# Kernel tuning notes

Measured on AMD Instinct MI355X. Metric: run time of the kernel, lower is better.

## Reference

```python
import jax, jax.numpy as jnp
import numpy as np

B, T, H, K = 64, 1024, 256, 4  # batch, seq_len, hidden_dim, crf_size


def setup_inputs() -> dict:
    key = jax.random.key(0)
    ks = jax.random.split(key, 8)
    return {
        "sentence_features": jax.random.normal(ks[0], (B, T, H), dtype=jnp.float32),
        "conv_w": jax.random.normal(ks[1], (H, H, 3), dtype=jnp.float32) * (1.0 / np.sqrt(3 * H)),
        "conv_b": jnp.zeros((H,), dtype=jnp.float32),
        "lin_w": jax.random.normal(ks[2], (K, H), dtype=jnp.float32) * (1.0 / np.sqrt(H)),
        "lin_b": jnp.zeros((K,), dtype=jnp.float32),
        "crf_start": jax.random.uniform(ks[3], (K,), dtype=jnp.float32, minval=-0.1, maxval=0.1),
        "crf_end": jax.random.uniform(ks[4], (K,), dtype=jnp.float32, minval=-0.1, maxval=0.1),
        "crf_trans": jax.random.uniform(ks[5], (K, K), dtype=jnp.float32, minval=-0.1, maxval=0.1),
    }


def _emissions(x, conv_w, conv_b, lin_w, lin_b):
    # x: [B, T, H] -> transpose -> Conv1d(k=3, pad=1) -> ReLU -> transpose -> Linear
    xc = jnp.swapaxes(x, 1, 2)  # [B, H, T]
    y = jax.lax.conv_general_dilated(
        xc, conv_w, window_strides=(1,), padding=((1, 1),),
        dimension_numbers=("NCH", "OIH", "NCH"))
    y = jax.nn.relu(y + conv_b[None, :, None])
    y = jnp.swapaxes(y, 1, 2)  # [B, T, H]
    return y @ lin_w.T + lin_b  # [B, T, K]


def _viterbi_decode(em, start, end, trans):
    # em: [B, T, K]; torchcrf CRF.decode with no mask (batch_first=True)
    score0 = start[None, :] + em[:, 0]  # [B, K]

    def step(score, emit_t):
        # score [B, K] over prev tag; broadcast to [B, K_prev, K_next]
        nxt = score[:, :, None] + trans[None, :, :] + emit_t[:, None, :]
        return jnp.max(nxt, axis=1), jnp.argmax(nxt, axis=1)  # new score, best prev tag

    em_rest = jnp.swapaxes(em[:, 1:], 0, 1)  # [T-1, B, K]
    final, history = jax.lax.scan(step, score0, em_rest)
    final = final + end[None, :]
    last_tag = jnp.argmax(final, axis=-1)  # [B]

    def back(tag, idx_t):
        prev = jnp.take_along_axis(idx_t, tag[:, None], axis=1)[:, 0]
        return prev, prev

    _, tags_head = jax.lax.scan(back, last_tag, history, reverse=True)  # [T-1, B]
    path = jnp.concatenate([jnp.swapaxes(tags_head, 0, 1), last_tag[:, None]], axis=1)
    return path.astype(jnp.int32)  # [B, T]


def reference(sentence_features, conv_w, conv_b, lin_w, lin_b, crf_start, crf_end, crf_trans):
    em = _emissions(sentence_features, conv_w, conv_b, lin_w, lin_b)
    return _viterbi_decode(em, crf_start, crf_end, crf_trans)
```

## Files before the change

kernel.cpp:

```cpp
#include <hip/hip_runtime.h>
#include <cstdint>
#include <cstddef>

typedef __attribute__((ext_vector_type(8))) short short8;
typedef __attribute__((ext_vector_type(4))) float f32x4;

constexpr int Bn = 64, Tn = 1024, Hn = 256, Kn = 4;
constexpr int TT = 128;
constexpr int AROWS = TT + 2;
constexpr int ARSTR = 144;

__device__ __forceinline__ unsigned bf16rne(float f) {
  unsigned u = __float_as_uint(f);
  return (u + 0x7fffu + ((u >> 16) & 1u)) >> 16;
}

__global__ __launch_bounds__(256) void pack_b_k(const float* __restrict__ conv_w,
                                                unsigned short* __restrict__ Bp) {
  int gt = blockIdx.x * 256 + threadIdx.x;
  int fid = gt >> 6, l = gt & 63;
  int ks = fid >> 5, rem = fid & 31;
  int p = rem >> 4, nf = rem & 15;
  int n = nf * 16 + (l & 15);
  int k0 = ks * 32 + ((l >> 4) << 3);
  short8 s;
  #pragma unroll
  for (int j = 0; j < 8; ++j) {
    int k = k0 + j;
    int dt = k >> 8, i = k & 255;
    float w = conv_w[n * 768 + i * 3 + dt];
    unsigned hb = bf16rne(w);
    if (p == 0) s[j] = (short)hb;
    else        s[j] = (short)bf16rne(w - __uint_as_float(hb << 16));
  }
  *reinterpret_cast<short8*>(Bp + (size_t)fid * 512 + l * 8) = s;
}

__global__ __launch_bounds__(256, 3) void emis_k(const float* __restrict__ x,
    const unsigned short* __restrict__ Bp, const float* __restrict__ conv_b,
    const float* __restrict__ lin_w, float* __restrict__ em2) {
  __shared__ __align__(16) char A_lds[AROWS * ARSTR];

  const int b = blockIdx.z, ny = blockIdx.y, t0 = blockIdx.x * TT;
  const int tid = threadIdx.x, lane = tid & 63, w = tid >> 6;
  const int wm = w >> 1, wn = w & 1;
  const float* xb = x + (size_t)b * Tn * Hn;

  auto stageA = [&](int ig) {
    #pragma unroll 1
    for (int it = 0; it < 5; ++it) {
      int idx = it * 256 + tid;
      if (idx < AROWS * 8) {
        int row = idx >> 3, c4 = idx & 7;
        int trow = t0 - 1 + row;
        float4 v = make_float4(0.f, 0.f, 0.f, 0.f);
        if (trow >= 0 && trow < Tn)
          v = *reinterpret_cast<const float4*>(xb + (size_t)trow * Hn + ig * 32 + c4 * 4);
        unsigned h[4], lo[4];
        float vf[4] = {v.x, v.y, v.z, v.w};
        #pragma unroll
        for (int q = 0; q < 4; ++q) {
          h[q] = bf16rne(vf[q]);
          lo[q] = bf16rne(vf[q] - __uint_as_float(h[q] << 16));
        }
        uint2 hp, lp;
        hp.x = h[0] | (h[1] << 16);  hp.y = h[2] | (h[3] << 16);
        lp.x = lo[0] | (lo[1] << 16); lp.y = lo[2] | (lo[3] << 16);
        char* base = A_lds + row * ARSTR + c4 * 8;
        *reinterpret_cast<uint2*>(base) = hp;
        *reinterpret_cast<uint2*>(base + 64) = lp;
      }
    }
  };

  const char* bsrc = reinterpret_cast<const char*>(Bp)
      + (size_t)(ny * 8 + wn * 4) * 1024 + lane * 16;
  auto loadB = [&](short8* Bh, short8* Bl, int ks) {
    #pragma unroll
    for (int nf = 0; nf < 4; ++nf) {
      Bh[nf] = *reinterpret_cast<const short8*>(bsrc + (size_t)((ks * 2 + 0) * 16 + nf) * 1024);
      Bl[nf] = *reinterpret_cast<const short8*>(bsrc + (size_t)((ks * 2 + 1) * 16 + nf) * 1024);
    }
  };

  f32x4 acc[4][4];
  #pragma unroll
  for (int mf = 0; mf < 4; ++mf)
    #pragma unroll
    for (int nf = 0; nf < 4; ++nf) acc[mf][nf] = (f32x4)0.f;

  const char* aB = A_lds + (lane & 15) * ARSTR + ((lane >> 4) << 4) + wm * 64 * ARSTR;

#define STEP(DT, BH, BL, NBH, NBL, KSN)                                       \
  {                                                                           \
    loadB(NBH, NBL, (KSN));                                                   \
    __builtin_amdgcn_s_setprio(1);                                            \
    _Pragma("unroll")                                                         \
    for (int mf = 0; mf < 4; ++mf) {                                          \
      const char* ap = aB + (mf * 16 + (DT)) * ARSTR;                         \
      short8 Ah = *reinterpret_cast<const short8*>(ap);                       \
      short8 Al = *reinterpret_cast<const short8*>(ap + 64);                  \
      _Pragma("unroll")                                                       \
      for (int nf = 0; nf < 4; ++nf) {                                        \
        f32x4 c = acc[mf][nf];                                                \
        c = __builtin_amdgcn_mfma_f32_16x16x32_bf16(Ah, BH[nf], c, 0, 0, 0);  \
        c = __builtin_amdgcn_mfma_f32_16x16x32_bf16(Al, BH[nf], c, 0, 0, 0);  \
        c = __builtin_amdgcn_mfma_f32_16x16x32_bf16(Ah, BL[nf], c, 0, 0, 0);  \
        acc[mf][nf] = c;                                                      \
      }                                                                       \
    }                                                                         \
    __builtin_amdgcn_s_setprio(0);                                            \
  }

  short8 BhA[4], BlA[4], BhB[4], BlB[4];
  loadB(BhA, BlA, 0);
  stageA(0);
  __syncthreads();

  #pragma unroll 1
  for (int igp = 0; igp < 4; ++igp) {
    const int ig0 = igp * 2, ig1 = ig0 + 1;
    STEP(0, BhA, BlA, BhB, BlB, 8 + ig0);
    STEP(1, BhB, BlB, BhA, BlA, 16 + ig0);
    STEP(2, BhA, BlA, BhB, BlB, ig1);
    __syncthreads();
    stageA(ig1);
    __syncthreads();
    STEP(0, BhB, BlB, BhA, BlA, 8 + ig1);
    STEP(1, BhA, BlA, BhB, BlB, 16 + ig1);
    STEP(2, BhB, BlB, BhA, BlA, (ig1 < 7 ? ig1 + 1 : 0));
    if (igp < 3) {
      __syncthreads();
      stageA(ig1 + 1);
      __syncthreads();
    }
  }
#undef STEP

  f32x4 pem[4][4];
  #pragma unroll
  for (int mf = 0; mf < 4; ++mf)
    #pragma unroll
    for (int v = 0; v < 4; ++v) pem[mf][v] = (f32x4)0.f;

  #pragma unroll
  for (int nf = 0; nf < 4; ++nf) {
    const int gcol = ny * 128 + wn * 64 + nf * 16 + (lane & 15);
    const float cb = conv_b[gcol];
    f32x4 lw;
    lw[0] = lin_w[gcol]; lw[1] = lin_w[256 + gcol];
    lw[2] = lin_w[512 + gcol]; lw[3] = lin_w[768 + gcol];
    #pragma unroll
    for (int mf = 0; mf < 4; ++mf)
      #pragma unroll
      for (int v = 0; v < 4; ++v) {
        float val = fmaxf(acc[mf][nf][v] + cb, 0.f);
        pem[mf][v] += val * lw;
      }
  }
  #pragma unroll
  for (int mf = 0; mf < 4; ++mf)
    #pragma unroll
    for (int v = 0; v < 4; ++v) {
      f32x4 t = pem[mf][v];
      #pragma unroll
      for (int m = 1; m < 16; m <<= 1) {
        f32x4 q;
        q[0] = __shfl_xor(t[0], m); q[1] = __shfl_xor(t[1], m);
        q[2] = __shfl_xor(t[2], m); q[3] = __shfl_xor(t[3], m);
        t += q;
      }
      pem[mf][v] = t;
    }
  __syncthreads();
  float* red = reinterpret_cast<float*>(A_lds);
  if ((lane & 15) == 0) {
    const int g = lane >> 4;
    #pragma unroll
    for (int mf = 0; mf < 4; ++mf)
      #pragma unroll
      for (int v = 0; v < 4; ++v) {
        int r = wm * 64 + mf * 16 + g * 4 + v;
        *reinterpret_cast<f32x4*>(red + (r * 2 + wn) * 4) = pem[mf][v];
      }
  }
  __syncthreads();
  if (tid < 128) {
    f32x4 s0 = *reinterpret_cast<f32x4*>(red + tid * 8);
    f32x4 s1 = *reinterpret_cast<f32x4*>(red + tid * 8 + 4);
    f32x4 s = s0 + s1;
    *reinterpret_cast<f32x4*>(em2 + ((size_t)(b * Tn + t0 + tid) * 2 + ny) * 4) = s;
  }
}

__device__ __forceinline__ unsigned int compose_map(unsigned int a, unsigned int b) {
#if __has_builtin(__builtin_amdgcn_perm)
  return __builtin_amdgcn_perm(a, a, b);
#else
  unsigned int c = 0;
  #pragma unroll
  for (int k = 0; k < 4; ++k) {
    unsigned int sel = (b >> (8 * k)) & 0xffu;
    c |= ((a >> (8 * sel)) & 0xffu) << (8 * k);
  }
  return c;
#endif
}

template <int J>
__device__ __forceinline__ float qb(float v) {
  return __int_as_float(__builtin_amdgcn_update_dpp(
      0, __float_as_int(v), (J * 0x55), 0xf, 0xf, true));
}

#define PSTEP(EV, T)                                                       \
  {                                                                        \
    shf[((T) - 1) * 4 + kk] = s;                                           \
    float c0 = qb<0>(s) + trc0;                                            \
    float c1 = qb<1>(s) + trc1;                                            \
    float c2 = qb<2>(s) + trc2;                                            \
    float c3 = qb<3>(s) + trc3;                                            \
    s = fmaxf(fmaxf(c0, c1), fmaxf(c2, c3)) + (EV);                        \
  }

__global__ __launch_bounds__(64) void viterbi_k(const float* __restrict__ em2,
    const float* __restrict__ lin_b, const float* __restrict__ cstart,
    const float* __restrict__ cend, const float* __restrict__ ctrans,
    int* __restrict__ out) {
  __shared__ float4 se[Tn];
  __shared__ float4 sh[Tn - 1];
  __shared__ int s_last;
  const int b = blockIdx.x, lane = threadIdx.x;
  const float4* e2 = reinterpret_cast<const float4*>(em2 + (size_t)b * Tn * 8);
  const float lb0 = lin_b[0], lb1 = lin_b[1], lb2 = lin_b[2], lb3 = lin_b[3];
  for (int i = lane; i < Tn; i += 64) {
    float4 a = e2[i * 2], c = e2[i * 2 + 1];
    se[i] = make_float4(a.x + c.x + lb0, a.y + c.y + lb1,
                        a.z + c.z + lb2, a.w + c.w + lb3);
  }
  float tr[4][4];
  #pragma unroll
  for (int j = 0; j < 4; ++j)
    #pragma unroll
    for (int k = 0; k < 4; ++k) tr[j][k] = ctrans[j * 4 + k];
  __syncthreads();

  if (lane < 4) {
    const int kk = lane;
    const float* sef = reinterpret_cast<const float*>(se);
    float* shf = reinterpret_cast<float*>(sh);
    const float trc0 = ctrans[0 * 4 + kk];
    const float trc1 = ctrans[1 * 4 + kk];
    const float trc2 = ctrans[2 * 4 + kk];
    const float trc3 = ctrans[3 * 4 + kk];
    float s = cstart[kk] + sef[kk];
    float e[8];
    #pragma unroll
    for (int d = 0; d < 8; ++d) e[d] = sef[(1 + d) * 4 + kk];
    int t = 1;
    #pragma unroll 1
    for (int g = 0; g < 127; ++g, t += 8) {
      float f[8];
      #pragma unroll
      for (int d = 0; d < 8; ++d) f[d] = e[d];
      #pragma unroll
      for (int d = 0; d < 8; ++d) e[d] = sef[(t + 8 + d) * 4 + kk];
      PSTEP(f[0], t);     PSTEP(f[1], t + 1);
      PSTEP(f[2], t + 2); PSTEP(f[3], t + 3);
      PSTEP(f[4], t + 4); PSTEP(f[5], t + 5);
      PSTEP(f[6], t + 6); PSTEP(f[7], t + 7);
    }
    PSTEP(e[0], 1017); PSTEP(e[1], 1018); PSTEP(e[2], 1019);
    PSTEP(e[3], 1020); PSTEP(e[4], 1021); PSTEP(e[5], 1022);
    PSTEP(e[6], 1023);
    s += cend[kk];
    float f0 = __shfl(s, 0), f1 = __shfl(s, 1);
    float f2 = __shfl(s, 2), f3 = __shfl(s, 3);
    if (kk == 0) {
      int tag = 0; float bf = f0;
      if (f1 > bf) { bf = f1; tag = 1; }
      if (f2 > bf) { bf = f2; tag = 2; }
      if (f3 > bf) { bf = f3; tag = 3; }
      s_last = tag;
    }
  }
  __syncthreads();

  const unsigned int ID = 0x03020100u;
  unsigned int mloc[16];
  const int t0 = lane * 16;
  #pragma unroll
  for (int k = 0; k < 16; ++k) {
    const int t = t0 + k;
    if (t < Tn - 1) {
      const float4 s = sh[t];
      const float4 e = se[t + 1];
      const float sj[4] = {s.x, s.y, s.z, s.w};
      const float ev[4] = {e.x, e.y, e.z, e.w};
      unsigned int mw = 0;
      #pragma unroll
      for (int kk = 0; kk < 4; ++kk) {
        float best = (sj[0] + tr[0][kk]) + ev[kk];
        int bi = 0;
        #pragma unroll
        for (int j = 1; j < 4; ++j) {
          float cc = (sj[j] + tr[j][kk]) + ev[kk];
          if (cc > best) { best = cc; bi = j; }
        }
        mw |= (unsigned)bi << (8 * kk);
      }
      mloc[k] = mw;
    } else {
      mloc[k] = ID;
    }
  }
  unsigned int P = mloc[15];
  #pragma unroll
  for (int k = 14; k >= 0; --k) P = compose_map(mloc[k], P);
  #pragma unroll
  for (int d = 1; d < 64; d <<= 1) {
    unsigned int q = (unsigned int)__shfl_down((int)P, d);
    if (lane + d > 63) q = ID;
    P = compose_map(P, q);
  }
  unsigned int E = (unsigned int)__shfl_down((int)P, 1);
  if (lane == 63) E = ID;
  const int last = s_last;
  unsigned int tag = (E >> (8 * last)) & 3u;
  int* ob = out + (size_t)b * Tn;
  #pragma unroll
  for (int k = 15; k >= 0; --k) {
    tag = (mloc[k] >> (8 * tag)) & 3u;
    ob[t0 + k] = (int)tag;
  }
}

extern "C" void kernel_launch(void* const* d_in, const int* in_sizes, int n_in,
                              void* d_out, int out_size, void* d_ws, size_t ws_size,
                              hipStream_t stream) {
  const float* x      = (const float*)d_in[0];
  const float* conv_w = (const float*)d_in[1];
  const float* conv_b = (const float*)d_in[2];
  const float* lin_w  = (const float*)d_in[3];
  const float* lin_b  = (const float*)d_in[4];
  const float* cstart = (const float*)d_in[5];
  const float* cend   = (const float*)d_in[6];
  const float* ctrans = (const float*)d_in[7];
  int* out = (int*)d_out;

  unsigned short* Bp = (unsigned short*)d_ws;
  float* em2 = (float*)((char*)d_ws + 786432);

  pack_b_k<<<192, 256, 0, stream>>>(conv_w, Bp);
  emis_k<<<dim3(Tn / TT, 2, Bn), 256, 0, stream>>>(x, Bp, conv_b, lin_w, em2);
  viterbi_k<<<Bn, 64, 0, stream>>>(em2, lin_b, cstart, cend, ctrans, out);
}
```

Before: 134.0 us.

## Double-buffer A tile in LDS and prefetch next slab into registers

Splits A staging into a global-to-register prefetch issued before the MFMA steps and a later register-to-LDS write into a second LDS buffer. This lets global loads of the next input slab overlap with matrix math and removes one of the two barriers per stage. The raw barrier waits only on LDS counters. It doubles the LDS footprint and holds more registers, and it lowers the launch-bounds occupancy hint from 3 to 2 blocks per SM.

```diff
diff --git a/kernel.cpp b/kernel.cpp
--- a/kernel.cpp
+++ b/kernel.cpp
@@ -9,6 +9,7 @@
 constexpr int TT = 128;
 constexpr int AROWS = TT + 2;
 constexpr int ARSTR = 144;
+constexpr int ABUFSZ = AROWS * ARSTR;
 
 __device__ __forceinline__ unsigned bf16rne(float f) {
   unsigned u = __float_as_uint(f);
@@ -36,18 +37,22 @@
   *reinterpret_cast<short8*>(Bp + (size_t)fid * 512 + l * 8) = s;
 }
 
-__global__ __launch_bounds__(256, 3) void emis_k(const float* __restrict__ x,
+#define GBAR() asm volatile("s_waitcnt lgkmcnt(0)\n\ts_barrier" ::: "memory")
+
+__global__ __launch_bounds__(256, 2) void emis_k(const float* __restrict__ x,
     const unsigned short* __restrict__ Bp, const float* __restrict__ conv_b,
     const float* __restrict__ lin_w, float* __restrict__ em2) {
-  __shared__ __align__(16) char A_lds[AROWS * ARSTR];
+  __shared__ __align__(16) char A_lds[2 * ABUFSZ];
 
   const int b = blockIdx.z, ny = blockIdx.y, t0 = blockIdx.x * TT;
   const int tid = threadIdx.x, lane = tid & 63, w = tid >> 6;
   const int wm = w >> 1, wn = w & 1;
   const float* xb = x + (size_t)b * Tn * Hn;
 
-  auto stageA = [&](int ig) {
-    #pragma unroll 1
+  float4 pre[5];
+
+  auto loadA = [&](int ig) {
+    #pragma unroll
     for (int it = 0; it < 5; ++it) {
       int idx = it * 256 + tid;
       if (idx < AROWS * 8) {
@@ -56,8 +61,18 @@
         float4 v = make_float4(0.f, 0.f, 0.f, 0.f);
         if (trow >= 0 && trow < Tn)
           v = *reinterpret_cast<const float4*>(xb + (size_t)trow * Hn + ig * 32 + c4 * 4);
+        pre[it] = v;
+      }
+    }
+  };
+  auto writeA = [&](int boff) {
+    #pragma unroll
+    for (int it = 0; it < 5; ++it) {
+      int idx = it * 256 + tid;
+      if (idx < AROWS * 8) {
+        int row = idx >> 3, c4 = idx & 7;
+        float vf[4] = {pre[it].x, pre[it].y, pre[it].z, pre[it].w};
         unsigned h[4], lo[4];
-        float vf[4] = {v.x, v.y, v.z, v.w};
         #pragma unroll
         for (int q = 0; q < 4; ++q) {
           h[q] = bf16rne(vf[q]);
@@ -66,7 +81,7 @@
         uint2 hp, lp;
         hp.x = h[0] | (h[1] << 16);  hp.y = h[2] | (h[3] << 16);
         lp.x = lo[0] | (lo[1] << 16); lp.y = lo[2] | (lo[3] << 16);
-        char* base = A_lds + row * ARSTR + c4 * 8;
+        char* base = A_lds + boff + row * ARSTR + c4 * 8;
         *reinterpret_cast<uint2*>(base) = hp;
         *reinterpret_cast<uint2*>(base + 64) = lp;
       }
@@ -91,13 +106,13 @@
 
   const char* aB = A_lds + (lane & 15) * ARSTR + ((lane >> 4) << 4) + wm * 64 * ARSTR;
 
-#define STEP(DT, BH, BL, NBH, NBL, KSN)                                       \
+#define STEP(ABUF, DT, BH, BL, NBH, NBL, KSN)                                 \
   {                                                                           \
     loadB(NBH, NBL, (KSN));                                                   \
     __builtin_amdgcn_s_setprio(1);                                            \
     _Pragma("unroll")                                                         \
     for (int mf = 0; mf < 4; ++mf) {                                          \
-      const char* ap = aB + (mf * 16 + (DT)) * ARSTR;                         \
+      const char* ap = aB + (ABUF) + (mf * 16 + (DT)) * ARSTR;                \
       short8 Ah = *reinterpret_cast<const short8*>(ap);                       \
       short8 Al = *reinterpret_cast<const short8*>(ap + 64);                  \
       _Pragma("unroll")                                                       \
@@ -113,27 +128,26 @@
   }
 
   short8 BhA[4], BlA[4], BhB[4], BlB[4];
+  loadA(0);
   loadB(BhA, BlA, 0);
-  stageA(0);
-  __syncthreads();
+  writeA(0);
+  GBAR();
 
   #pragma unroll 1
   for (int igp = 0; igp < 4; ++igp) {
     const int ig0 = igp * 2, ig1 = ig0 + 1;
-    STEP(0, BhA, BlA, BhB, BlB, 8 + ig0);
-    STEP(1, BhB, BlB, BhA, BlA, 16 + ig0);
-    STEP(2, BhA, BlA, BhB, BlB, ig1);
-    __syncthreads();
-    stageA(ig1);
-    __syncthreads();
-    STEP(0, BhB, BlB, BhA, BlA, 8 + ig1);
-    STEP(1, BhA, BlA, BhB, BlB, 16 + ig1);
-    STEP(2, BhB, BlB, BhA, BlA, (ig1 < 7 ? ig1 + 1 : 0));
-    if (igp < 3) {
-      __syncthreads();
-      stageA(ig1 + 1);
-      __syncthreads();
-    }
+    loadA(ig1);
+    STEP(0, 0, BhA, BlA, BhB, BlB, 8 + ig0);
+    STEP(0, 1, BhB, BlB, BhA, BlA, 16 + ig0);
+    STEP(0, 2, BhA, BlA, BhB, BlB, ig1);
+    writeA(ABUFSZ);
+    GBAR();
+    if (ig1 < 7) loadA(ig1 + 1);
+    STEP(ABUFSZ, 0, BhB, BlB, BhA, BlA, 8 + ig1);
+    STEP(ABUFSZ, 1, BhA, BlA, BhB, BlB, 16 + ig1);
+    STEP(ABUFSZ, 2, BhB, BlB, BhA, BlA, (ig1 < 7 ? ig1 + 1 : 0));
+    if (ig1 < 7) writeA(0);
+    GBAR();
   }
 #undef STEP
 
```

Measured after the change: 123.4 us. -7.9%, faster.
